# Kernel optimization log

Measured on AMD Instinct MI355X. Metric: run time of the kernel, lower is better.

The kernel has to match this reference:

```python
import jax, jax.numpy as jnp
import numpy as np

B, P, D_MODEL = 16, 256, 1024
V, D_LLM = 1000, 4096
H, DK = 16, 64  # d_keys = d_model // n_heads


def setup_inputs() -> dict:
    key = jax.random.key(0)
    ks = jax.random.split(key, 11)
    s = lambda k, shape, fan: jax.random.normal(k, shape, jnp.float32) / np.sqrt(fan)
    return {
        "target_embedding": jax.random.normal(ks[0], (B, P, D_MODEL), jnp.float32),
        "source_embedding": jax.random.normal(ks[1], (V, D_LLM), jnp.float32),
        "value_embedding": jax.random.normal(ks[2], (V, D_LLM), jnp.float32),
        "Wq": s(ks[3], (D_MODEL, H * DK), D_MODEL),
        "bq": jnp.zeros((H * DK,), jnp.float32),
        "Wk": s(ks[4], (D_LLM, H * DK), D_LLM),
        "bk": jnp.zeros((H * DK,), jnp.float32),
        "Wv": s(ks[5], (D_LLM, H * DK), D_LLM),
        "bv": jnp.zeros((H * DK,), jnp.float32),
        "Wo": s(ks[6], (H * DK, D_LLM), H * DK),
        "bo": jnp.zeros((D_LLM,), jnp.float32),
    }


def reference(target_embedding, source_embedding, value_embedding,
              Wq, bq, Wk, bk, Wv, bv, Wo, bo):
    b, p, _ = target_embedding.shape
    v = source_embedding.shape[0]
    # projections
    Q = (target_embedding @ Wq + bq).reshape(b, p, H, DK)   # bphd
    K = (source_embedding @ Wk + bk).reshape(v, H, DK)      # vhd
    Vv = (value_embedding @ Wv + bv).reshape(v, H, DK)      # vhd
    scale = 1.0 / np.sqrt(DK)
    # NOTE: non-standard einsum — contracts over v, elementwise in d
    scores = jnp.einsum('bphd,vhd->bhpd', Q, K)             # [B,H,P,DK]
    A = jax.nn.softmax(scale * scores, axis=-1)             # softmax over head dim d
    # (dropout is identity in eval mode)
    R = jnp.einsum('bhpd,vhd->bphd', A, Vv)                 # A * sum_v V
    out = R.reshape(b, p, H * DK) @ Wo + bo                 # [B,P,D_LLM]
    return out
```

## Files before the change

kernel.cpp:

```cpp
#include <hip/hip_runtime.h>

#define BB   16
#define PP   256
#define BP   4096
#define DMODEL 1024
#define VV   1000
#define DLLM 4096
#define HH   16
#define DK   64
#define HDK  1024

using f32x4 = __attribute__((ext_vector_type(4))) float;
using s16x8 = __attribute__((ext_vector_type(8))) short;
using us8   = __attribute__((ext_vector_type(8))) unsigned short;

__device__ __forceinline__ unsigned short f2bf(float f) {
    unsigned int u = __builtin_bit_cast(unsigned int, f);
    u = (u + 0x7FFFu + ((u >> 16) & 1u)) >> 16;
    return (unsigned short)u;
}

__device__ __forceinline__ void gload_lds16(const unsigned short* g, unsigned short* lds) {
    __builtin_amdgcn_global_load_lds(
        (const __attribute__((address_space(1))) void*)g,
        (__attribute__((address_space(3))) void*)lds,
        16, 0, 0);
}

__device__ __forceinline__ void transpose_body(const float* __restrict__ src,
                                               unsigned short* __restrict__ dst,
                                               int R, int C, int bx, int by, int t,
                                               float (*tile)[33]) {
    int x = t & 7, y = t >> 3;
    int c0 = bx * 32, r0 = by * 32;
    float4 v = *reinterpret_cast<const float4*>(&src[(size_t)(r0 + y) * C + c0 + x * 4]);
    tile[y][x * 4 + 0] = v.x; tile[y][x * 4 + 1] = v.y;
    tile[y][x * 4 + 2] = v.z; tile[y][x * 4 + 3] = v.w;
    __syncthreads();
    ushort4 o = make_ushort4(f2bf(tile[x * 4 + 0][y]), f2bf(tile[x * 4 + 1][y]),
                             f2bf(tile[x * 4 + 2][y]), f2bf(tile[x * 4 + 3][y]));
    *reinterpret_cast<ushort4*>(&dst[(size_t)(c0 + y) * R + r0 + x * 4]) = o;
}

__global__ void mega1(const float* __restrict__ src0, const float* __restrict__ src1,
                      float* __restrict__ part1,
                      const float* __restrict__ target, unsigned short* __restrict__ tgt_bf,
                      const float* __restrict__ Wq, unsigned short* __restrict__ wq_t,
                      const float* __restrict__ Wo, unsigned short* __restrict__ wo_t) {
    __shared__ float tile[32][33];
    int b = blockIdx.x, t = threadIdx.x;
    if (b < 320) {
        int z = b / 160, rem = b % 160, y = rem >> 2, x = rem & 3;
        int col4 = x * 256 + t;
        const float4* src = reinterpret_cast<const float4*>(z ? src1 : src0);
        int r0 = y * 25;
        float4 acc = make_float4(0.f, 0.f, 0.f, 0.f);
        for (int r = 0; r < 25; ++r) {
            float4 v = src[(size_t)(r0 + r) * (DLLM / 4) + col4];
            acc.x += v.x; acc.y += v.y; acc.z += v.z; acc.w += v.w;
        }
        reinterpret_cast<float4*>(part1)[(size_t)(z * 40 + y) * (DLLM / 4) + col4] = acc;
    } else if (b < 320 + 2048) {
        int idx = (b - 320) * 256 + t;
        float4 v0 = reinterpret_cast<const float4*>(target)[idx * 2];
        float4 v1 = reinterpret_cast<const float4*>(target)[idx * 2 + 1];
        us8 o = { f2bf(v0.x), f2bf(v0.y), f2bf(v0.z), f2bf(v0.w),
                  f2bf(v1.x), f2bf(v1.y), f2bf(v1.z), f2bf(v1.w) };
        *reinterpret_cast<us8*>(&tgt_bf[(size_t)idx * 8]) = o;
    } else if (b < 320 + 2048 + 1024) {
        int b2 = b - 2368;
        transpose_body(Wq, wq_t, DMODEL, HDK, b2 & 31, b2 >> 5, t, tile);
    } else {
        int b2 = b - 3392;
        transpose_body(Wo, wo_t, HDK, DLLM, b2 & 127, b2 >> 7, t, tile);
    }
}

__global__ void gemv_partial2(const float* __restrict__ Wk, const float* __restrict__ Wv,
                              const float* __restrict__ part1, float* __restrict__ part2) {
    __shared__ float vec[64];
    int c     = blockIdx.x * 256 + threadIdx.x;
    int chunk = blockIdx.y;
    int z     = blockIdx.z;
    const float* W = z ? Wv : Wk;
    if (threadIdx.x < 64) {
        int r = chunk * 64 + threadIdx.x;
        float a = 0.f;
        for (int p = 0; p < 40; ++p)
            a += part1[(size_t)(z * 40 + p) * DLLM + r];
        vec[threadIdx.x] = a;
    }
    __syncthreads();
    float acc = 0.f;
    int r0 = chunk * 64;
    for (int r = 0; r < 64; ++r)
        acc += vec[r] * W[(size_t)(r0 + r) * HDK + c];
    part2[((z * 64 + chunk) * HDK) + c] = acc;
}

__global__ void gemv_reduce(const float* __restrict__ part,
                            const float* __restrict__ bk, const float* __restrict__ bv,
                            float* __restrict__ kvsum) {
    int idx = blockIdx.x * 256 + threadIdx.x;
    int z = idx >> 10, c = idx & 1023;
    float acc = 0.f;
    for (int ch = 0; ch < 64; ++ch) acc += part[(size_t)(z * 64 + ch) * HDK + c];
    acc += (float)VV * (z ? bv[c] : bk[c]);
    kvsum[idx] = acc;
}

template<int EPI, int BMt, int BNt, int WM, int WN, int BMPX, int NXBN, int BNPX>
__global__ __launch_bounds__(WM * WN * 64, 2)
void gemm_ctd3(const unsigned short* __restrict__ A, const unsigned short* __restrict__ Bt,
               float* __restrict__ C, const float* __restrict__ bias,
               const float* __restrict__ kvsum, unsigned short* __restrict__ R,
               int N, int K) {
    constexpr int WAVES = WM * WN;
    constexpr int Mw = BMt / WM;
    constexpr int M_REP = Mw / 16;
    constexpr int NA = BMt * 32 / (WAVES * 512);
    constexpr int NB = BNt * 32 / (WAVES * 512);
    constexpr int NST = NA + NB;
    static_assert(BNt / WN == 64, "wave col span must be 64");
    static_assert(NA >= 1 && NB >= 1, "staging geometry");

    __shared__ __align__(16) unsigned short Asm[3][BMt * 32];
    __shared__ __align__(16) unsigned short Bsm[3][BNt * 32];

    const int xcd = blockIdx.x & 7, l = blockIdx.x >> 3;
    const int bm = ((xcd / NXBN) * BMPX + (l % BMPX)) * BMt;
    const int bn = ((xcd % NXBN) * BNPX + (l / BMPX)) * BNt;

    const int t = threadIdx.x;
    const int w = t >> 6, lane = t & 63;
    const int wr = w / WN, wc = w % WN;
    const int l15 = lane & 15, kgrp = lane >> 4;

    size_t goffA[NA], goffB[NB];
    int ldsoA[NA], ldsoB[NB];
    {
        int s8 = lane & 7, jj = lane >> 3;
#pragma unroll
        for (int i = 0; i < NA; ++i) {
            int sr = (i * WAVES + w) * 8 + jj;
            int x = s8 ^ (sr & 7);
            goffA[i] = (size_t)(bm + sr * 2 + (x >> 2)) * K + (x & 3) * 8;
            ldsoA[i] = (i * WAVES + w) * 512;
        }
#pragma unroll
        for (int i = 0; i < NB; ++i) {
            int sr = (i * WAVES + w) * 8 + jj;
            int x = s8 ^ (sr & 7);
            goffB[i] = (size_t)(bn + sr * 2 + (x >> 2)) * K + (x & 3) * 8;
            ldsoB[i] = (i * WAVES + w) * 512;
        }
    }
    int ra[M_REP], rb[4];
#pragma unroll
    for (int m = 0; m < M_REP; ++m) {
        int r = wr * Mw + m * 16 + l15;
        int s8 = (kgrp + 4 * (r & 1)) ^ ((r >> 1) & 7);
        ra[m] = (r >> 1) * 64 + s8 * 8;
    }
#pragma unroll
    for (int n = 0; n < 4; ++n) {
        int r = wc * 64 + n * 16 + l15;
        int s8 = (kgrp + 4 * (r & 1)) ^ ((r >> 1) & 7);
        rb[n] = (r >> 1) * 64 + s8 * 8;
    }

    f32x4 acc[M_REP][4] = {};

#define STAGE(t_, b_) do { size_t k0_ = (size_t)(t_) * 32;             \
    _Pragma("unroll")                                                  \
    for (int i_ = 0; i_ < NA; ++i_)                                    \
        gload_lds16(A + goffA[i_] + k0_, &Asm[b_][ldsoA[i_]]);         \
    _Pragma("unroll")                                                  \
    for (int i_ = 0; i_ < NB; ++i_)                                    \
        gload_lds16(Bt + goffB[i_] + k0_, &Bsm[b_][ldsoB[i_]]); } while (0)

#define WAIT_NST() do {                                                 \
    if constexpr (NST == 6) asm volatile("s_waitcnt vmcnt(6)" ::: "memory"); \
    else if constexpr (NST == 4) asm volatile("s_waitcnt vmcnt(4)" ::: "memory"); \
    else if constexpr (NST == 3) asm volatile("s_waitcnt vmcnt(3)" ::: "memory"); \
    else asm volatile("s_waitcnt vmcnt(2)" ::: "memory"); } while (0)

    const int nT = K >> 5;
    STAGE(0, 0); STAGE(1, 1);
    WAIT_NST();
    __builtin_amdgcn_s_barrier();

    int cur = 0;
    for (int tk = 0; tk < nT; ++tk) {
        s16x8 af[M_REP], bfr[4];
#pragma unroll
        for (int m = 0; m < M_REP; ++m)
            af[m] = *reinterpret_cast<const s16x8*>(&Asm[cur][ra[m]]);
#pragma unroll
        for (int n = 0; n < 4; ++n)
            bfr[n] = *reinterpret_cast<const s16x8*>(&Bsm[cur][rb[n]]);
        if (tk + 2 < nT) STAGE(tk + 2, cur == 0 ? 2 : cur - 1);
        __builtin_amdgcn_s_setprio(1);
#pragma unroll
        for (int m = 0; m < M_REP; ++m)
#pragma unroll
            for (int n = 0; n < 4; ++n)
                acc[m][n] = __builtin_amdgcn_mfma_f32_16x16x32_bf16(af[m], bfr[n], acc[m][n], 0, 0, 0);
        __builtin_amdgcn_s_setprio(0);
        if (tk + 2 < nT) {
            WAIT_NST();
        } else if (tk + 1 < nT) {
            asm volatile("s_waitcnt vmcnt(0)" ::: "memory");
        }
        if (tk + 1 < nT) __builtin_amdgcn_s_barrier();
        cur = (cur == 2) ? 0 : cur + 1;
    }
#undef STAGE
#undef WAIT_NST

    if (EPI == 0) {
#pragma unroll
        for (int m = 0; m < M_REP; ++m) {
            int grow = bm + wr * Mw + m * 16 + kgrp * 4;
#pragma unroll
            for (int n = 0; n < 4; ++n) {
                int gcol = bn + wc * 64 + n * 16 + l15;
                float bb = bias[gcol];
#pragma unroll
                for (int j = 0; j < 4; ++j)
                    C[(size_t)(grow + j) * N + gcol] = acc[m][n][j] + bb;
            }
        }
    } else {
        float bqv[4], ksv[4], vsv[4];
#pragma unroll
        for (int n = 0; n < 4; ++n) {
            int col = bn + wc * 64 + n * 16 + l15;
            bqv[n] = bias[col];
            ksv[n] = kvsum[col];
            vsv[n] = kvsum[HDK + col];
        }
#pragma unroll
        for (int m = 0; m < M_REP; ++m) {
            int grow = bm + wr * Mw + m * 16 + kgrp * 4;
#pragma unroll
            for (int j = 0; j < 4; ++j) {
                float x[4];
#pragma unroll
                for (int n = 0; n < 4; ++n)
                    x[n] = 0.125f * (acc[m][n][j] + bqv[n]) * ksv[n];
                float mx = fmaxf(fmaxf(x[0], x[1]), fmaxf(x[2], x[3]));
#pragma unroll
                for (int off = 8; off; off >>= 1) mx = fmaxf(mx, __shfl_xor(mx, off));
                float e[4], s = 0.f;
#pragma unroll
                for (int n = 0; n < 4; ++n) { e[n] = __expf(x[n] - mx); s += e[n]; }
#pragma unroll
                for (int off = 8; off; off >>= 1) s += __shfl_xor(s, off);
                float inv = 1.0f / s;
#pragma unroll
                for (int n = 0; n < 4; ++n) {
                    int col = bn + wc * 64 + n * 16 + l15;
                    R[(size_t)(grow + j) * N + col] = f2bf(e[n] * inv * vsv[n]);
                }
            }
        }
    }
}

extern "C" void kernel_launch(void* const* d_in, const int* in_sizes, int n_in,
                              void* d_out, int out_size, void* d_ws, size_t ws_size,
                              hipStream_t stream) {
    const float* target = (const float*)d_in[0];
    const float* source = (const float*)d_in[1];
    const float* value  = (const float*)d_in[2];
    const float* Wq = (const float*)d_in[3];
    const float* bq = (const float*)d_in[4];
    const float* Wk = (const float*)d_in[5];
    const float* bk = (const float*)d_in[6];
    const float* Wv = (const float*)d_in[7];
    const float* bv = (const float*)d_in[8];
    const float* Wo = (const float*)d_in[9];
    const float* bo = (const float*)d_in[10];
    float* out = (float*)d_out;

    char* ws = (char*)d_ws;
    float*          part1  = (float*)(ws);
    float*          part2  = (float*)(ws + 0x180000);
    float*          kvsum  = (float*)(ws + 0x210000);
    unsigned short* tgt_bf = (unsigned short*)(ws + 0x400000);
    unsigned short* wq_t   = (unsigned short*)(ws + 0xC00000);
    unsigned short* wo_t   = (unsigned short*)(ws + 0xE00000);
    unsigned short* Rb     = (unsigned short*)(ws + 0x1600000);

    mega1<<<7488, 256, 0, stream>>>(source, value, part1, target, tgt_bf, Wq, wq_t, Wo, wo_t);

    gemv_partial2<<<dim3(4, 64, 2), 256, 0, stream>>>(Wk, Wv, part1, part2);
    gemv_reduce<<<8, 256, 0, stream>>>(part2, bk, bv, kvsum);

    gemm_ctd3<1, 64, 128, 2, 2, 16, 2, 4><<<512, 256, 0, stream>>>(
        tgt_bf, wq_t, nullptr, bq, kvsum, Rb, HDK, DMODEL);

    gemm_ctd3<0, 256, 128, 2, 2, 8, 4, 8><<<512, 256, 0, stream>>>(
        Rb, wo_t, out, bo, nullptr, nullptr, DLLM, HDK);
}
```

Before: 93.15 us.

## Load B operand directly to registers in output GEMM, stage only A in LDS

Adds a new gemm_bd kernel for the final Wo projection. It keeps the A tile (R activations) in a triple-buffered LDS pipeline but loads each wave's B fragments straight from global memory into registers, double-buffered across an unrolled-by-two K loop. This cuts LDS footprint and LDS read traffic for B, which could allow more overlap or occupancy. The cost is uncoalesced-ish per-lane 16-byte global loads of B and more vector registers. The old gemm_ctd3 is reduced to the softmax epilogue only.

```diff
diff --git a/kernel.cpp b/kernel.cpp
--- a/kernel.cpp
+++ b/kernel.cpp
@@ -26,6 +26,8 @@
         (__attribute__((address_space(3))) void*)lds,
         16, 0, 0);
 }
+
+#define WAITVM(n_) asm volatile("s_waitcnt vmcnt(%0)" :: "n"(n_) : "memory")
 
 __device__ __forceinline__ void transpose_body(const float* __restrict__ src,
                                                unsigned short* __restrict__ dst,
@@ -122,7 +124,6 @@
     constexpr int NB = BNt * 32 / (WAVES * 512);
     constexpr int NST = NA + NB;
     static_assert(BNt / WN == 64, "wave col span must be 64");
-    static_assert(NA >= 1 && NB >= 1, "staging geometry");
 
     __shared__ __align__(16) unsigned short Asm[3][BMt * 32];
     __shared__ __align__(16) unsigned short Bsm[3][BNt * 32];
@@ -171,7 +172,7 @@
 
     f32x4 acc[M_REP][4] = {};
 
-#define STAGE(t_, b_) do { size_t k0_ = (size_t)(t_) * 32;             \
+#define STG(t_, b_) do { size_t k0_ = (size_t)(t_) * 32;               \
     _Pragma("unroll")                                                  \
     for (int i_ = 0; i_ < NA; ++i_)                                    \
         gload_lds16(A + goffA[i_] + k0_, &Asm[b_][ldsoA[i_]]);         \
@@ -179,15 +180,9 @@
     for (int i_ = 0; i_ < NB; ++i_)                                    \
         gload_lds16(Bt + goffB[i_] + k0_, &Bsm[b_][ldsoB[i_]]); } while (0)
 
-#define WAIT_NST() do {                                                 \
-    if constexpr (NST == 6) asm volatile("s_waitcnt vmcnt(6)" ::: "memory"); \
-    else if constexpr (NST == 4) asm volatile("s_waitcnt vmcnt(4)" ::: "memory"); \
-    else if constexpr (NST == 3) asm volatile("s_waitcnt vmcnt(3)" ::: "memory"); \
-    else asm volatile("s_waitcnt vmcnt(2)" ::: "memory"); } while (0)
-
     const int nT = K >> 5;
-    STAGE(0, 0); STAGE(1, 1);
-    WAIT_NST();
+    STG(0, 0); STG(1, 1);
+    WAITVM(NST);
     __builtin_amdgcn_s_barrier();
 
     int cur = 0;
@@ -199,7 +194,7 @@
 #pragma unroll
         for (int n = 0; n < 4; ++n)
             bfr[n] = *reinterpret_cast<const s16x8*>(&Bsm[cur][rb[n]]);
-        if (tk + 2 < nT) STAGE(tk + 2, cur == 0 ? 2 : cur - 1);
+        if (tk + 2 < nT) STG(tk + 2, cur == 0 ? 2 : cur - 1);
         __builtin_amdgcn_s_setprio(1);
 #pragma unroll
         for (int m = 0; m < M_REP; ++m)
@@ -207,63 +202,164 @@
             for (int n = 0; n < 4; ++n)
                 acc[m][n] = __builtin_amdgcn_mfma_f32_16x16x32_bf16(af[m], bfr[n], acc[m][n], 0, 0, 0);
         __builtin_amdgcn_s_setprio(0);
-        if (tk + 2 < nT) {
-            WAIT_NST();
-        } else if (tk + 1 < nT) {
-            asm volatile("s_waitcnt vmcnt(0)" ::: "memory");
-        }
+        if (tk + 2 < nT)      WAITVM(NST);
+        else if (tk + 1 < nT) WAITVM(0);
         if (tk + 1 < nT) __builtin_amdgcn_s_barrier();
         cur = (cur == 2) ? 0 : cur + 1;
     }
-#undef STAGE
-#undef WAIT_NST
-
-    if (EPI == 0) {
-#pragma unroll
-        for (int m = 0; m < M_REP; ++m) {
-            int grow = bm + wr * Mw + m * 16 + kgrp * 4;
+#undef STG
+
+    float bqv[4], ksv[4], vsv[4];
+#pragma unroll
+    for (int n = 0; n < 4; ++n) {
+        int col = bn + wc * 64 + n * 16 + l15;
+        bqv[n] = bias[col];
+        ksv[n] = kvsum[col];
+        vsv[n] = kvsum[HDK + col];
+    }
+#pragma unroll
+    for (int m = 0; m < M_REP; ++m) {
+        int grow = bm + wr * Mw + m * 16 + kgrp * 4;
+#pragma unroll
+        for (int j = 0; j < 4; ++j) {
+            float x[4];
+#pragma unroll
+            for (int n = 0; n < 4; ++n)
+                x[n] = 0.125f * (acc[m][n][j] + bqv[n]) * ksv[n];
+            float mx = fmaxf(fmaxf(x[0], x[1]), fmaxf(x[2], x[3]));
+#pragma unroll
+            for (int off = 8; off; off >>= 1) mx = fmaxf(mx, __shfl_xor(mx, off));
+            float e[4], s = 0.f;
+#pragma unroll
+            for (int n = 0; n < 4; ++n) { e[n] = __expf(x[n] - mx); s += e[n]; }
+#pragma unroll
+            for (int off = 8; off; off >>= 1) s += __shfl_xor(s, off);
+            float inv = 1.0f / s;
 #pragma unroll
             for (int n = 0; n < 4; ++n) {
-                int gcol = bn + wc * 64 + n * 16 + l15;
-                float bb = bias[gcol];
-#pragma unroll
-                for (int j = 0; j < 4; ++j)
-                    C[(size_t)(grow + j) * N + gcol] = acc[m][n][j] + bb;
+                int col = bn + wc * 64 + n * 16 + l15;
+                R[(size_t)(grow + j) * N + col] = f2bf(e[n] * inv * vsv[n]);
             }
         }
-    } else {
-        float bqv[4], ksv[4], vsv[4];
+    }
+}
+
+template<int BMt, int BNt, int WM, int WN, int BMPX, int NXBN, int BNPX>
+__global__ __launch_bounds__(WM * WN * 64, 2)
+void gemm_bd(const unsigned short* __restrict__ A, const unsigned short* __restrict__ Bt,
+             float* __restrict__ C, const float* __restrict__ bias, int N, int K) {
+    constexpr int WAVES = WM * WN;
+    constexpr int Mw = BMt / WM;
+    constexpr int M_REP = Mw / 16;
+    constexpr int NA = BMt * 32 / (WAVES * 512);
+    static_assert(BNt / WN == 64, "wave col span must be 64");
+    static_assert(NA == 4, "wait counts below assume NA == 4");
+
+    __shared__ __align__(16) unsigned short Asm[3][BMt * 32];
+
+    const int xcd = blockIdx.x & 7, l = blockIdx.x >> 3;
+    const int bm = ((xcd / NXBN) * BMPX + (l % BMPX)) * BMt;
+    const int bn = ((xcd % NXBN) * BNPX + (l / BMPX)) * BNt;
+
+    const int t = threadIdx.x;
+    const int w = t >> 6, lane = t & 63;
+    const int wr = w / WN, wc = w % WN;
+    const int l15 = lane & 15, kgrp = lane >> 4;
+
+    size_t goffA[NA];
+    int ldsoA[NA];
+    {
+        int s8 = lane & 7, jj = lane >> 3;
+#pragma unroll
+        for (int i = 0; i < NA; ++i) {
+            int sr = (i * WAVES + w) * 8 + jj;
+            int x = s8 ^ (sr & 7);
+            goffA[i] = (size_t)(bm + sr * 2 + (x >> 2)) * K + (x & 3) * 8;
+            ldsoA[i] = (i * WAVES + w) * 512;
+        }
+    }
+    int ra[M_REP];
+#pragma unroll
+    for (int m = 0; m < M_REP; ++m) {
+        int r = wr * Mw + m * 16 + l15;
+        int s8 = (kgrp + 4 * (r & 1)) ^ ((r >> 1) & 7);
+        ra[m] = (r >> 1) * 64 + s8 * 8;
+    }
+    size_t gBoff[4];
+#pragma unroll
+    for (int n = 0; n < 4; ++n)
+        gBoff[n] = (size_t)(bn + wc * 64 + n * 16 + l15) * K + kgrp * 8;
+
+    f32x4 acc[M_REP][4] = {};
+    s16x8 bf0[4], bf1[4];
+
+#define STAGE_A(t_, b_) do { size_t k0_ = (size_t)(t_) * 32;           \
+    _Pragma("unroll")                                                  \
+    for (int i_ = 0; i_ < NA; ++i_)                                    \
+        gload_lds16(A + goffA[i_] + k0_, &Asm[b_][ldsoA[i_]]); } while (0)
+
+#define LOADB(bf_, t_) do { _Pragma("unroll")                          \
+    for (int n_ = 0; n_ < 4; ++n_)                                     \
+        bf_[n_] = *reinterpret_cast<const s16x8*>(&Bt[gBoff[n_] + (size_t)(t_) * 32]); } while (0)
+
+#define READA(b_) do { _Pragma("unroll")                               \
+    for (int m_ = 0; m_ < M_REP; ++m_)                                 \
+        af[m_] = *reinterpret_cast<const s16x8*>(&Asm[b_][ra[m_]]); } while (0)
+
+#define MFMAS(bf_) do {                                                \
+    __builtin_amdgcn_s_setprio(1);                                     \
+    _Pragma("unroll")                                                  \
+    for (int m_ = 0; m_ < M_REP; ++m_)                                 \
+        _Pragma("unroll")                                              \
+        for (int n_ = 0; n_ < 4; ++n_)                                 \
+            acc[m_][n_] = __builtin_amdgcn_mfma_f32_16x16x32_bf16(     \
+                af[m_], bf_[n_], acc[m_][n_], 0, 0, 0);                \
+    __builtin_amdgcn_s_setprio(0); } while (0)
+
+    const int nT = K >> 5;
+    s16x8 af[M_REP];
+
+    LOADB(bf0, 0);
+    STAGE_A(0, 0); STAGE_A(1, 1);
+    WAITVM(4);
+    __builtin_amdgcn_s_barrier();
+
+    int cur = 0;
+    for (int tk = 0; tk < nT; tk += 2) {
+        READA(cur);
+        if (tk + 1 < nT) LOADB(bf1, tk + 1);
+        if (tk + 2 < nT) STAGE_A(tk + 2, cur == 0 ? 2 : cur - 1);
+        MFMAS(bf0);
+        if (tk + 1 < nT) {
+            if (tk + 2 < nT) WAITVM(8); else WAITVM(4);
+            __builtin_amdgcn_s_barrier();
+        }
+        cur = (cur == 2) ? 0 : cur + 1;
+        READA(cur);
+        if (tk + 2 < nT) LOADB(bf0, tk + 2);
+        if (tk + 3 < nT) STAGE_A(tk + 3, cur == 0 ? 2 : cur - 1);
+        MFMAS(bf1);
+        if (tk + 2 < nT) {
+            if (tk + 3 < nT) WAITVM(8); else WAITVM(4);
+            __builtin_amdgcn_s_barrier();
+        }
+        cur = (cur == 2) ? 0 : cur + 1;
+    }
+#undef STAGE_A
+#undef LOADB
+#undef READA
+#undef MFMAS
+
+#pragma unroll
+    for (int m = 0; m < M_REP; ++m) {
+        int grow = bm + wr * Mw + m * 16 + kgrp * 4;
 #pragma unroll
         for (int n = 0; n < 4; ++n) {
-            int col = bn + wc * 64 + n * 16 + l15;
-            bqv[n] = bias[col];
-            ksv[n] = kvsum[col];
-            vsv[n] = kvsum[HDK + col];
-        }
-#pragma unroll
-        for (int m = 0; m < M_REP; ++m) {
-            int grow = bm + wr * Mw + m * 16 + kgrp * 4;
-#pragma unroll
-            for (int j = 0; j < 4; ++j) {
-                float x[4];
-#pragma unroll
-                for (int n = 0; n < 4; ++n)
-                    x[n] = 0.125f * (acc[m][n][j] + bqv[n]) * ksv[n];
-                float mx = fmaxf(fmaxf(x[0], x[1]), fmaxf(x[2], x[3]));
-#pragma unroll
-                for (int off = 8; off; off >>= 1) mx = fmaxf(mx, __shfl_xor(mx, off));
-                float e[4], s = 0.f;
-#pragma unroll
-                for (int n = 0; n < 4; ++n) { e[n] = __expf(x[n] - mx); s += e[n]; }
-#pragma unroll
-                for (int off = 8; off; off >>= 1) s += __shfl_xor(s, off);
-                float inv = 1.0f / s;
-#pragma unroll
-                for (int n = 0; n < 4; ++n) {
-                    int col = bn + wc * 64 + n * 16 + l15;
-                    R[(size_t)(grow + j) * N + col] = f2bf(e[n] * inv * vsv[n]);
-                }
-            }
+            int gcol = bn + wc * 64 + n * 16 + l15;
+            float bb = bias[gcol];
+#pragma unroll
+            for (int j = 0; j < 4; ++j)
+                C[(size_t)(grow + j) * N + gcol] = acc[m][n][j] + bb;
         }
     }
 }
@@ -301,6 +397,6 @@
     gemm_ctd3<1, 64, 128, 2, 2, 16, 2, 4><<<512, 256, 0, stream>>>(
         tgt_bf, wq_t, nullptr, bq, kvsum, Rb, HDK, DMODEL);
 
-    gemm_ctd3<0, 256, 128, 2, 2, 8, 4, 8><<<512, 256, 0, stream>>>(
-        Rb, wo_t, out, bo, nullptr, nullptr, DLLM, HDK);
-}
+    gemm_bd<256, 128, 2, 2, 8, 4, 8><<<512, 256, 0, stream>>>(
+        Rb, wo_t, out, bo, DLLM, HDK);
+}
```

Result: slower. 105.5 us (+13.2%).
